# Optimization experiments

Measured on AMD Instinct MI355X. Metric: run time of the kernel, lower is better.

## Reference

```python
import jax, jax.numpy as jnp
import numpy as np

NUM_HEADS = 16


def setup_inputs() -> dict:
    key = jax.random.key(0)
    ks = jax.random.split(key, 5)
    N, L, E = 4, 1024, 1024
    x = jax.random.normal(ks[0], (N, L, E), dtype=jnp.float32)
    sc = 1.0 / np.sqrt(E)
    wq = jax.random.normal(ks[1], (E, E), dtype=jnp.float32) * sc
    wk = jax.random.normal(ks[2], (E, E), dtype=jnp.float32) * sc
    wv = jax.random.normal(ks[3], (E, E), dtype=jnp.float32) * sc
    wo = jax.random.normal(ks[4], (E, E), dtype=jnp.float32) * sc
    return {"x": x, "wq": wq, "wk": wk, "wv": wv, "wo": wo}


def reference(x, wq, wk, wv, wo):
    N, L, E = x.shape
    H = NUM_HEADS
    d = E // H  # d_k = d_v = d_q
    # Linear layers: y = x @ W^T (torch Linear weight is (out, in))
    q = (x @ wq.T).reshape(N, H, L, d)  # NOTE: raw view, matches torch .view
    k = (x @ wk.T).reshape(N, H, L, d)
    v = (x @ wv.T).reshape(N, H, L, d)
    scores = jnp.einsum("nhld,nhmd->nhlm", q, k) / jnp.sqrt(jnp.float32(d))
    # causal mask (dropout is identity in eval / p=0)
    causal = jnp.tril(jnp.ones((L, L), dtype=bool))
    scores = jnp.where(causal, scores, jnp.float32(-jnp.inf))
    attn = jax.nn.softmax(scores, axis=-1)
    wei = jnp.einsum("nhlm,nhmd->nhld", attn, v).reshape(N, L, H * d)
    return wei @ wo.T
```

## Files before the change

### kernel.cpp

```cpp
#include <hip/hip_runtime.h>
#include <hip/hip_bf16.h>

using bf16 = __hip_bfloat16;
typedef __attribute__((ext_vector_type(8))) short bf16x8;
typedef __attribute__((ext_vector_type(4))) float f32x4;

#define MFMA16(a, b, c) __builtin_amdgcn_mfma_f32_16x16x32_bf16(a, b, c, 0, 0, 0)
#define SWZ(row, byteoff) ((byteoff) ^ (((row) & 7) << 4))

__device__ __forceinline__ unsigned short f2b(float f) {
  union { float f; unsigned int u; } c; c.f = f;
  unsigned int r = c.u + 0x7fffu + ((c.u >> 16) & 1u);
  return (unsigned short)(r >> 16);
}
__device__ __forceinline__ float b2f(short b) {
  union { unsigned int u; float f; } c;
  c.u = ((unsigned int)(unsigned short)b) << 16;
  return c.f;
}
__device__ __forceinline__ bf16x8 scale8(bf16x8 v, float s) {
  bf16x8 r;
#pragma unroll
  for (int j = 0; j < 8; ++j) r[j] = (short)f2b(b2f(v[j]) * s);
  return r;
}

__device__ __forceinline__ void gload_lds16(const void* g, void* l) {
  __builtin_amdgcn_global_load_lds(
      (const __attribute__((address_space(1))) void*)g,
      (__attribute__((address_space(3))) void*)l, 16, 0, 0);
}

__device__ __forceinline__ void store_out(float* p, float v) { *p = v; }
__device__ __forceinline__ void store_out(bf16* p, float v) {
  *(unsigned short*)p = f2b(v);
}

__global__ __launch_bounds__(256) void cast_all(
    const float* __restrict__ x, const float* __restrict__ wq,
    const float* __restrict__ wk, const float* __restrict__ wv,
    const float* __restrict__ wo,
    unsigned short* __restrict__ xb, unsigned short* __restrict__ wqb,
    unsigned short* __restrict__ wkb, unsigned short* __restrict__ wvb,
    unsigned short* __restrict__ wob) {
  int i = blockIdx.x * 256 + threadIdx.x;
  const float* src;
  unsigned short* dst;
  int off;
  if (i < 1048576) {
    src = x; dst = xb; off = i;
  } else {
    int j = i - 1048576;
    int seg = j >> 18;
    off = j & 262143;
    src = (seg == 0) ? wq : (seg == 1) ? wk : (seg == 2) ? wv : wo;
    dst = (seg == 0) ? wqb : (seg == 1) ? wkb : (seg == 2) ? wvb : wob;
  }
  float4 v = reinterpret_cast<const float4*>(src)[off];
  ushort4 o;
  o.x = f2b(v.x); o.y = f2b(v.y); o.z = f2b(v.z); o.w = f2b(v.w);
  reinterpret_cast<ushort4*>(dst)[off] = o;
}

template <typename TOUT>
__device__ __forceinline__ void gemm_tile(const bf16* __restrict__ A,
                                          const bf16* __restrict__ Bt,
                                          TOUT* __restrict__ C, int N, int K,
                                          int bm, int bn) {
  __shared__ bf16 Asm[128 * 32];
  __shared__ bf16 Bsm[128 * 32];
  const int tid = threadIdx.x;
  const int lane = tid & 63;
  const int w = tid >> 6;
  const int wr = w >> 1, wc = w & 1;
  const int fr = lane & 15;
  const int fk = (lane >> 4) * 8;
  f32x4 acc[4][4] = {};

  const int srow = w * 16 + (lane >> 2);
  const int scol = (lane & 3) * 8;
  const bf16* Ag = A + (size_t)(bm + srow) * K + scol;
  const bf16* Bg = Bt + (size_t)srow * K + scol;
  bf16* AsW = &Asm[(w * 16) * 32];
  bf16* BsW = &Bsm[(w * 16) * 32];

  for (int kt = 0; kt < K; kt += 32) {
    gload_lds16(Ag + kt, AsW);
    gload_lds16(Ag + kt + (size_t)64 * K, AsW + 64 * 32);
    gload_lds16(Bg + kt, BsW);
    gload_lds16(Bg + kt + (size_t)64 * K, BsW + 64 * 32);
    __syncthreads();
    bf16x8 afr[4], bfr[4];
#pragma unroll
    for (int m = 0; m < 4; ++m)
      afr[m] = *(const bf16x8*)&Asm[(wr * 64 + m * 16 + fr) * 32 + fk];
#pragma unroll
    for (int n = 0; n < 4; ++n)
      bfr[n] = *(const bf16x8*)&Bsm[(wc * 64 + n * 16 + fr) * 32 + fk];
#pragma unroll
    for (int m = 0; m < 4; ++m)
#pragma unroll
      for (int n = 0; n < 4; ++n)
        acc[m][n] = MFMA16(afr[m], bfr[n], acc[m][n]);
    __syncthreads();
  }
#pragma unroll
  for (int m = 0; m < 4; ++m) {
    const int row0 = bm + wr * 64 + m * 16 + (lane >> 4) * 4;
#pragma unroll
    for (int n = 0; n < 4; ++n) {
      const int col = bn + wc * 64 + n * 16 + fr;
#pragma unroll
      for (int r = 0; r < 4; ++r)
        store_out(&C[(size_t)(row0 + r) * N + col], acc[m][n][r]);
    }
  }
}

__global__ __launch_bounds__(256) void gemm_qkv(
    const bf16* __restrict__ A, const bf16* __restrict__ B3,
    bf16* __restrict__ Cq, bf16* __restrict__ Ck, bf16* __restrict__ Cv) {
  const int bm = blockIdx.x * 128;
  const int bnG = blockIdx.y * 128;
  bf16* C = (bnG < 1024) ? Cq : (bnG < 2048) ? Ck : Cv;
  gemm_tile<bf16>(A, B3 + (size_t)bnG * 1024, C, 1024, 1024, bm, bnG & 1023);
}

__global__ __launch_bounds__(256) void gemm_out(const bf16* __restrict__ A,
                                                const bf16* __restrict__ B,
                                                float* __restrict__ C) {
  gemm_tile<float>(A, B + (size_t)blockIdx.y * 128 * 1024, C, 1024, 1024,
                   blockIdx.x * 128, blockIdx.y * 128);
}

__global__ __launch_bounds__(256) void attn_fwd(
    const bf16* __restrict__ Q, const bf16* __restrict__ K,
    const bf16* __restrict__ V, bf16* __restrict__ O) {
  const int nh = blockIdx.y;
  const size_t base = (size_t)nh * 65536;
  const bf16* Qp = Q + base;
  const bf16* Kp = K + base;
  const bf16* Vp = V + base;
  bf16* Op = O + base;
  const int p = blockIdx.x;
  const int qiA = p, qiB = 15 - p;
  const int tid = threadIdx.x;
  const int lane = tid & 63;
  const int w = tid >> 6;
  const int fr = lane & 15;
  const int fg = lane >> 4;

  __shared__ bf16 Ksm[2][64 * 64];
  __shared__ bf16 Vts[2][64 * 64];
  __shared__ bf16 Psm[4][2][16 * 64];

  const float QSC = 0.125f * 1.44269504089f;
  const float MS = 12.0f;
  const int rA0 = qiA * 64 + w * 16;
  const int rB0 = qiB * 64 + w * 16;
  bf16x8 qA[2], qB[2];
#pragma unroll
  for (int ks = 0; ks < 2; ++ks) {
    qA[ks] = scale8(
        *(const bf16x8*)&Qp[(size_t)(rA0 + fr) * 64 + ks * 32 + fg * 8], QSC);
    qB[ks] = scale8(
        *(const bf16x8*)&Qp[(size_t)(rB0 + fr) * 64 + ks * 32 + fg * 8], QSC);
  }

  float sA[4] = {0.f, 0.f, 0.f, 0.f};
  float sB[4] = {0.f, 0.f, 0.f, 0.f};
  f32x4 oA[4], oB[4];
#pragma unroll
  for (int d = 0; d < 4; ++d) {
    oA[d] = (f32x4){0.f, 0.f, 0.f, 0.f};
    oB[d] = (f32x4){0.f, 0.f, 0.f, 0.f};
  }

  const int NKV = qiB + 1;

  const int bkv = (tid & 15) * 4;
  const int bd = (tid >> 4) * 4;
  union VU { ushort4 v; unsigned short s[4]; };
  VU v4[4], nv4[4];

  const int krow = w * 16 + (lane >> 3);
  const int kcb = (lane & 7) * 16;

#define STAGE_K(kt, bi)                                                       \
  {                                                                           \
    _Pragma("unroll") for (int i = 0; i < 2; ++i) {                           \
      const int row = krow + i * 8;                                           \
      gload_lds16((const char*)Kp + ((size_t)((kt)*64 + row) * 128 +          \
                                     SWZ(row, kcb)),                          \
                  (char*)&Ksm[bi][0] + (w * 16 + i * 8) * 128);               \
    }                                                                         \
  }
#define LOAD_V(kt, r)                                                         \
  {                                                                           \
    _Pragma("unroll") for (int j = 0; j < 4; ++j) (r)[j].v =                  \
        *(const ushort4*)(Vp + (size_t)((kt)*64 + bkv + j) * 64 + bd);        \
  }
#define WRITE_V(bi, r)                                                        \
  {                                                                           \
    _Pragma("unroll") for (int i = 0; i < 4; ++i) {                           \
      VU o4;                                                                  \
      _Pragma("unroll") for (int j = 0; j < 4; ++j) o4.s[j] = (r)[j].s[i];    \
      const int row = bd + i;                                                 \
      *(ushort4*)((char*)&Vts[bi][0] + row * 128 + SWZ(row, bkv * 2)) = o4.v; \
    }                                                                         \
  }

  STAGE_K(0, 0);
  LOAD_V(0, v4);
  WRITE_V(0, v4);
  __syncthreads();

  for (int kt = 0; kt < NKV; ++kt) {
    const int b = kt & 1;
    const bool more = (kt + 1 < NKV);
    if (more) {
      STAGE_K(kt + 1, b ^ 1);
      LOAD_V(kt + 1, nv4);
    }
    const bool aAct = (kt <= qiA);

    bf16x8 kf[4][2];
#pragma unroll
    for (int c = 0; c < 4; ++c) {
      const int row = c * 16 + fr;
      const char* rp = (const char*)&Ksm[b][0] + row * 128;
      kf[c][0] = *(const bf16x8*)(rp + SWZ(row, fg * 16));
      kf[c][1] = *(const bf16x8*)(rp + SWZ(row, 64 + fg * 16));
    }

    auto strip_sm = [&](const bf16x8 (&qf)[2], float (&s)[4], bf16* Pw,
                        bool diag, int qrow0, bf16x8 (&pf)[2]) {
      f32x4 sc[4];
      __builtin_amdgcn_s_setprio(1);
#pragma unroll
      for (int c = 0; c < 4; ++c) {
        f32x4 acc = (f32x4){0.f, 0.f, 0.f, 0.f};
        acc = MFMA16(qf[0], kf[c][0], acc);
        acc = MFMA16(qf[1], kf[c][1], acc);
        sc[c] = acc;
      }
      __builtin_amdgcn_s_setprio(0);
#pragma unroll
      for (int c = 0; c < 4; ++c)
#pragma unroll
        for (int r = 0; r < 4; ++r) {
          float sv = sc[c][r];
          if (diag) {
            const int kcol = c * 16 + fr;
            const int qrow = qrow0 + r;
            sv = (kcol <= qrow) ? sv : -INFINITY;
          }
          const float e = __builtin_amdgcn_exp2f(sv - MS);
          s[r] += e;
          const int row = fg * 4 + r;
          *(unsigned short*)((char*)Pw + row * 128 +
                             SWZ(row, (c * 16 + fr) * 2)) = f2b(e);
        }
#pragma unroll
      for (int ks = 0; ks < 2; ++ks)
        pf[ks] = *(const bf16x8*)((char*)Pw + fr * 128 +
                                  SWZ(fr, ks * 64 + fg * 16));
    };

    bf16x8 pfA[2], pfB[2];
    strip_sm(qB, sB, &Psm[w][1][0], kt == qiB, w * 16 + fg * 4, pfB);
    if (aAct) strip_sm(qA, sA, &Psm[w][0][0], kt == qiA, w * 16 + fg * 4, pfA);

    bf16x8 vf[4][2];
#pragma unroll
    for (int d = 0; d < 4; ++d) {
      const int row = d * 16 + fr;
      const char* rp = (const char*)&Vts[b][0] + row * 128;
      vf[d][0] = *(const bf16x8*)(rp + SWZ(row, fg * 16));
      vf[d][1] = *(const bf16x8*)(rp + SWZ(row, 64 + fg * 16));
    }
    __builtin_amdgcn_s_setprio(1);
#pragma unroll
    for (int d = 0; d < 4; ++d) {
      oB[d] = MFMA16(pfB[0], vf[d][0], oB[d]);
      oB[d] = MFMA16(pfB[1], vf[d][1], oB[d]);
    }
    if (aAct) {
#pragma unroll
      for (int d = 0; d < 4; ++d) {
        oA[d] = MFMA16(pfA[0], vf[d][0], oA[d]);
        oA[d] = MFMA16(pfA[1], vf[d][1], oA[d]);
      }
    }
    __builtin_amdgcn_s_setprio(0);

    if (more) WRITE_V(b ^ 1, nv4);
    __syncthreads();
  }

#pragma unroll
  for (int msk = 1; msk <= 8; msk <<= 1)
#pragma unroll
    for (int r = 0; r < 4; ++r) {
      sA[r] += __shfl_xor(sA[r], msk);
      sB[r] += __shfl_xor(sB[r], msk);
    }

#pragma unroll
  for (int d = 0; d < 4; ++d)
#pragma unroll
    for (int r = 0; r < 4; ++r) {
      const float vA = oA[d][r] / sA[r];
      const float vB = oB[d][r] / sB[r];
      *(unsigned short*)&Op[(size_t)(rA0 + fg * 4 + r) * 64 + d * 16 + fr] =
          f2b(vA);
      *(unsigned short*)&Op[(size_t)(rB0 + fg * 4 + r) * 64 + d * 16 + fr] =
          f2b(vB);
    }
#undef STAGE_K
#undef LOAD_V
#undef WRITE_V
}

extern "C" void kernel_launch(void* const* d_in, const int* in_sizes, int n_in,
                              void* d_out, int out_size, void* d_ws,
                              size_t ws_size, hipStream_t stream) {
  const float* x = (const float*)d_in[0];
  const float* wq = (const float*)d_in[1];
  const float* wk = (const float*)d_in[2];
  const float* wv = (const float*)d_in[3];
  const float* wo = (const float*)d_in[4];
  float* out = (float*)d_out;
  char* ws = (char*)d_ws;

  bf16* xb = (bf16*)(ws);
  bf16* wqkv = (bf16*)(ws + (8u << 20));
  bf16* wqb = wqkv;
  bf16* wkb = (bf16*)(ws + (10u << 20));
  bf16* wvb = (bf16*)(ws + (12u << 20));
  bf16* wob = (bf16*)(ws + (14u << 20));
  bf16* qbuf = (bf16*)(ws + (16u << 20));
  bf16* kbuf = (bf16*)(ws + (24u << 20));
  bf16* vbuf = (bf16*)(ws + (32u << 20));
  bf16* weib = (bf16*)(ws);

  cast_all<<<8192, 256, 0, stream>>>(x, wq, wk, wv, wo, (unsigned short*)xb,
                                     (unsigned short*)wqb, (unsigned short*)wkb,
                                     (unsigned short*)wvb, (unsigned short*)wob);
  gemm_qkv<<<dim3(32, 24), 256, 0, stream>>>(xb, wqkv, qbuf, kbuf, vbuf);
  attn_fwd<<<dim3(8, 64), 256, 0, stream>>>(qbuf, kbuf, vbuf, weib);
  gemm_out<<<dim3(32, 8), 256, 0, stream>>>(weib, wob, out);
}
```

Measured before the change: 102.0 us.

## Replace QKV GEMM with 256x256-tile, 512-thread, triple-buffered pipelined kernel

The QKV projection now uses a new kernel with 256x256 output tiles, 8 waves per block and a 3-stage LDS ring fed by direct global-to-LDS loads. Waits use explicit vmcnt counts and raised MFMA priority so loads overlap compute. The larger tiles raise operand reuse and cut global traffic. In exchange the grid shrinks from 768 to 192 blocks on a GPU with many CUs, which risks poor occupancy and load balance, and LDS use grows to 96 KB per block.

```diff
diff --git a/kernel.cpp b/kernel.cpp
--- a/kernel.cpp
+++ b/kernel.cpp
@@ -7,6 +7,7 @@
 
 #define MFMA16(a, b, c) __builtin_amdgcn_mfma_f32_16x16x32_bf16(a, b, c, 0, 0, 0)
 #define SWZ(row, byteoff) ((byteoff) ^ (((row) & 7) << 4))
+#define SWZ64(row, byteoff) ((byteoff) ^ (((row) & 3) << 4))
 
 __device__ __forceinline__ unsigned short f2b(float f) {
   union { float f; unsigned int u; } c; c.f = f;
@@ -117,20 +118,116 @@
   }
 }
 
-__global__ __launch_bounds__(256) void gemm_qkv(
-    const bf16* __restrict__ A, const bf16* __restrict__ B3,
-    bf16* __restrict__ Cq, bf16* __restrict__ Ck, bf16* __restrict__ Cv) {
-  const int bm = blockIdx.x * 128;
-  const int bnG = blockIdx.y * 128;
-  bf16* C = (bnG < 1024) ? Cq : (bnG < 2048) ? Ck : Cv;
-  gemm_tile<bf16>(A, B3 + (size_t)bnG * 1024, C, 1024, 1024, bm, bnG & 1023);
-}
-
 __global__ __launch_bounds__(256) void gemm_out(const bf16* __restrict__ A,
                                                 const bf16* __restrict__ B,
                                                 float* __restrict__ C) {
   gemm_tile<float>(A, B + (size_t)blockIdx.y * 128 * 1024, C, 1024, 1024,
                    blockIdx.x * 128, blockIdx.y * 128);
+}
+
+__global__ __launch_bounds__(512, 2) void gemm_qkv_256(
+    const bf16* __restrict__ A, const bf16* __restrict__ B3,
+    bf16* __restrict__ Cq, bf16* __restrict__ Ck, bf16* __restrict__ Cv) {
+  __shared__ bf16 Ab[3][256 * 32];
+  __shared__ bf16 Bb[3][256 * 32];
+  const int tid = threadIdx.x;
+  const int lane = tid & 63;
+  const int w = tid >> 6;
+  const int wr = w >> 2;
+  const int wc = w & 3;
+  const int fr = lane & 15;
+  const int fg = lane >> 4;
+  const int bm = blockIdx.x * 256;
+  const int bnG = blockIdx.y * 256;
+  const bf16* Bt = B3 + (size_t)bnG * 1024;
+  bf16* C = (bnG < 1024) ? Cq : (bnG < 2048) ? Ck : Cv;
+  const int bn = bnG & 1023;
+
+  const int sr = w * 16 + (lane >> 2);
+  const int scb = (lane & 3) * 16;
+
+  f32x4 acc[8][4] = {};
+
+#define STAGE256(kt, s)                                                      \
+  {                                                                          \
+    const size_t kc = (size_t)(kt) * 32;                                     \
+    _Pragma("unroll") for (int ra = 0; ra < 2; ++ra) {                       \
+      const int row = ra * 128 + sr;                                         \
+      gload_lds16((const char*)(A + (size_t)(bm + row) * 1024 + kc) +        \
+                      SWZ64(row, scb),                                       \
+                  (char*)&Ab[s][0] + (ra * 128 + w * 16) * 64);              \
+      gload_lds16((const char*)(Bt + (size_t)row * 1024 + kc) +              \
+                      SWZ64(row, scb),                                       \
+                  (char*)&Bb[s][0] + (ra * 128 + w * 16) * 64);              \
+    }                                                                        \
+  }
+
+#define COMPUTE256(s)                                                        \
+  {                                                                          \
+    bf16x8 af[8];                                                            \
+    _Pragma("unroll") for (int m = 0; m < 8; ++m) {                          \
+      const int row = wr * 128 + m * 16 + fr;                                \
+      af[m] = *(const bf16x8*)((const char*)&Ab[s][0] + row * 64 +           \
+                               SWZ64(row, fg * 16));                         \
+    }                                                                        \
+    _Pragma("unroll") for (int nh = 0; nh < 2; ++nh) {                       \
+      bf16x8 bfv[2];                                                         \
+      _Pragma("unroll") for (int n = 0; n < 2; ++n) {                        \
+        const int row = wc * 64 + (nh * 2 + n) * 16 + fr;                    \
+        bfv[n] = *(const bf16x8*)((const char*)&Bb[s][0] + row * 64 +        \
+                                  SWZ64(row, fg * 16));                      \
+      }                                                                      \
+      __builtin_amdgcn_s_setprio(1);                                         \
+      _Pragma("unroll") for (int m = 0; m < 8; ++m)                          \
+          _Pragma("unroll") for (int n = 0; n < 2; ++n) acc[m][nh * 2 + n] = \
+              MFMA16(af[m], bfv[n], acc[m][nh * 2 + n]);                     \
+      __builtin_amdgcn_s_setprio(0);                                         \
+    }                                                                        \
+  }
+
+  STAGE256(0, 0);
+  STAGE256(1, 1);
+  STAGE256(2, 2);
+  __builtin_amdgcn_sched_barrier(0);
+  asm volatile("s_waitcnt vmcnt(8)" ::: "memory");
+  __builtin_amdgcn_s_barrier();
+  __builtin_amdgcn_sched_barrier(0);
+
+  int s = 0;
+  for (int t = 0; t < 32; ++t) {
+    COMPUTE256(s);
+    __builtin_amdgcn_sched_barrier(0);
+    __builtin_amdgcn_s_barrier();
+    __builtin_amdgcn_sched_barrier(0);
+    if (t + 3 < 32) {
+      STAGE256(t + 3, s);
+      __builtin_amdgcn_sched_barrier(0);
+      asm volatile("s_waitcnt vmcnt(8)" ::: "memory");
+    } else if (t + 2 < 32) {
+      asm volatile("s_waitcnt vmcnt(4)" ::: "memory");
+    } else if (t + 1 < 32) {
+      asm volatile("s_waitcnt vmcnt(0)" ::: "memory");
+    }
+    if (t + 1 < 32) {
+      __builtin_amdgcn_s_barrier();
+      __builtin_amdgcn_sched_barrier(0);
+    }
+    s = (s == 2) ? 0 : s + 1;
+  }
+
+#pragma unroll
+  for (int m = 0; m < 8; ++m) {
+    const int row0 = bm + wr * 128 + m * 16 + fg * 4;
+#pragma unroll
+    for (int n = 0; n < 4; ++n) {
+      const int col = bn + wc * 64 + n * 16 + fr;
+#pragma unroll
+      for (int r = 0; r < 4; ++r)
+        store_out(&C[(size_t)(row0 + r) * 1024 + col], acc[m][n][r]);
+    }
+  }
+#undef STAGE256
+#undef COMPUTE256
 }
 
 __global__ __launch_bounds__(256) void attn_fwd(
@@ -347,7 +444,7 @@
   cast_all<<<8192, 256, 0, stream>>>(x, wq, wk, wv, wo, (unsigned short*)xb,
                                      (unsigned short*)wqb, (unsigned short*)wkb,
                                      (unsigned short*)wvb, (unsigned short*)wob);
-  gemm_qkv<<<dim3(32, 24), 256, 0, stream>>>(xb, wqkv, qbuf, kbuf, vbuf);
+  gemm_qkv_256<<<dim3(16, 12), 512, 0, stream>>>(xb, wqkv, qbuf, kbuf, vbuf);
   attn_fwd<<<dim3(8, 64), 256, 0, stream>>>(qbuf, kbuf, vbuf, weib);
   gemm_out<<<dim3(32, 8), 256, 0, stream>>>(weib, wob, out);
 }
```

Result: slower. 115.9 us (+13.6%).

## Process four causal query strips per attention block to reuse K/V tiles

Applied to the files above, without the earlier changes.

Each attention block now handles four query strips (g, 7-g, 8+g, 15-g) instead of two, so every staged K/V tile in LDS feeds up to four strips' MFMAs. This halves the grid to 4x64 blocks and halves redundant K/V global loads per head, while keeping the causal work balanced across blocks. The cost is more registers per thread (four sets of Q fragments and accumulators), which the launch bound of one block per CU accommodates, and fewer blocks (256) to fill the GPU's CUs.

```diff
diff --git a/kernel.cpp b/kernel.cpp
--- a/kernel.cpp
+++ b/kernel.cpp
@@ -133,7 +133,7 @@
                    blockIdx.x * 128, blockIdx.y * 128);
 }
 
-__global__ __launch_bounds__(256) void attn_fwd(
+__global__ __launch_bounds__(256, 1) void attn_fwd(
     const bf16* __restrict__ Q, const bf16* __restrict__ K,
     const bf16* __restrict__ V, bf16* __restrict__ O) {
   const int nh = blockIdx.y;
@@ -142,8 +142,8 @@
   const bf16* Kp = K + base;
   const bf16* Vp = V + base;
   bf16* Op = O + base;
-  const int p = blockIdx.x;
-  const int qiA = p, qiB = 15 - p;
+  const int g = blockIdx.x;
+  const int strips[4] = {g, 7 - g, 8 + g, 15 - g};
   const int tid = threadIdx.x;
   const int lane = tid & 63;
   const int w = tid >> 6;
@@ -152,31 +152,32 @@
 
   __shared__ bf16 Ksm[2][64 * 64];
   __shared__ bf16 Vts[2][64 * 64];
-  __shared__ bf16 Psm[4][2][16 * 64];
+  __shared__ bf16 Psm[4][4][16 * 64];
 
   const float QSC = 0.125f * 1.44269504089f;
   const float MS = 12.0f;
-  const int rA0 = qiA * 64 + w * 16;
-  const int rB0 = qiB * 64 + w * 16;
-  bf16x8 qA[2], qB[2];
-#pragma unroll
-  for (int ks = 0; ks < 2; ++ks) {
-    qA[ks] = scale8(
-        *(const bf16x8*)&Qp[(size_t)(rA0 + fr) * 64 + ks * 32 + fg * 8], QSC);
-    qB[ks] = scale8(
-        *(const bf16x8*)&Qp[(size_t)(rB0 + fr) * 64 + ks * 32 + fg * 8], QSC);
-  }
-
-  float sA[4] = {0.f, 0.f, 0.f, 0.f};
-  float sB[4] = {0.f, 0.f, 0.f, 0.f};
-  f32x4 oA[4], oB[4];
-#pragma unroll
-  for (int d = 0; d < 4; ++d) {
-    oA[d] = (f32x4){0.f, 0.f, 0.f, 0.f};
-    oB[d] = (f32x4){0.f, 0.f, 0.f, 0.f};
-  }
-
-  const int NKV = qiB + 1;
+
+  bf16x8 qf[4][2];
+#pragma unroll
+  for (int si = 0; si < 4; ++si) {
+    const int r0 = strips[si] * 64 + w * 16;
+#pragma unroll
+    for (int ks = 0; ks < 2; ++ks)
+      qf[si][ks] = scale8(
+          *(const bf16x8*)&Qp[(size_t)(r0 + fr) * 64 + ks * 32 + fg * 8], QSC);
+  }
+
+  float sm[4][4];
+  f32x4 o[4][4];
+#pragma unroll
+  for (int si = 0; si < 4; ++si)
+#pragma unroll
+    for (int r = 0; r < 4; ++r) {
+      sm[si][r] = 0.f;
+      o[si][r] = (f32x4){0.f, 0.f, 0.f, 0.f};
+    }
+
+  const int NKV = strips[3] + 1;
 
   const int bkv = (tid & 15) * 4;
   const int bd = (tid >> 4) * 4;
@@ -222,7 +223,6 @@
       STAGE_K(kt + 1, b ^ 1);
       LOAD_V(kt + 1, nv4);
     }
-    const bool aAct = (kt <= qiA);
 
     bf16x8 kf[4][2];
 #pragma unroll
@@ -233,15 +233,15 @@
       kf[c][1] = *(const bf16x8*)(rp + SWZ(row, 64 + fg * 16));
     }
 
-    auto strip_sm = [&](const bf16x8 (&qf)[2], float (&s)[4], bf16* Pw,
+    auto strip_sm = [&](const bf16x8 (&qfs)[2], float (&s)[4], bf16* Pw,
                         bool diag, int qrow0, bf16x8 (&pf)[2]) {
       f32x4 sc[4];
       __builtin_amdgcn_s_setprio(1);
 #pragma unroll
       for (int c = 0; c < 4; ++c) {
         f32x4 acc = (f32x4){0.f, 0.f, 0.f, 0.f};
-        acc = MFMA16(qf[0], kf[c][0], acc);
-        acc = MFMA16(qf[1], kf[c][1], acc);
+        acc = MFMA16(qfs[0], kf[c][0], acc);
+        acc = MFMA16(qfs[1], kf[c][1], acc);
         sc[c] = acc;
       }
       __builtin_amdgcn_s_setprio(0);
@@ -267,9 +267,13 @@
                                   SWZ(fr, ks * 64 + fg * 16));
     };
 
-    bf16x8 pfA[2], pfB[2];
-    strip_sm(qB, sB, &Psm[w][1][0], kt == qiB, w * 16 + fg * 4, pfB);
-    if (aAct) strip_sm(qA, sA, &Psm[w][0][0], kt == qiA, w * 16 + fg * 4, pfA);
+    bf16x8 pf[4][2];
+    const int qrow0 = w * 16 + fg * 4;
+#pragma unroll
+    for (int si = 0; si < 4; ++si)
+      if (kt <= strips[si])
+        strip_sm(qf[si], sm[si], &Psm[w][si][0], kt == strips[si], qrow0,
+                 pf[si]);
 
     bf16x8 vf[4][2];
 #pragma unroll
@@ -281,17 +285,14 @@
     }
     __builtin_amdgcn_s_setprio(1);
 #pragma unroll
-    for (int d = 0; d < 4; ++d) {
-      oB[d] = MFMA16(pfB[0], vf[d][0], oB[d]);
-      oB[d] = MFMA16(pfB[1], vf[d][1], oB[d]);
-    }
-    if (aAct) {
-#pragma unroll
-      for (int d = 0; d < 4; ++d) {
-        oA[d] = MFMA16(pfA[0], vf[d][0], oA[d]);
-        oA[d] = MFMA16(pfA[1], vf[d][1], oA[d]);
+    for (int si = 0; si < 4; ++si)
+      if (kt <= strips[si]) {
+#pragma unroll
+        for (int d = 0; d < 4; ++d) {
+          o[si][d] = MFMA16(pf[si][0], vf[d][0], o[si][d]);
+          o[si][d] = MFMA16(pf[si][1], vf[d][1], o[si][d]);
+        }
       }
-    }
     __builtin_amdgcn_s_setprio(0);
 
     if (more) WRITE_V(b ^ 1, nv4);
@@ -301,22 +302,22 @@
 #pragma unroll
   for (int msk = 1; msk <= 8; msk <<= 1)
 #pragma unroll
-    for (int r = 0; r < 4; ++r) {
-      sA[r] += __shfl_xor(sA[r], msk);
-      sB[r] += __shfl_xor(sB[r], msk);
-    }
-
-#pragma unroll
-  for (int d = 0; d < 4; ++d)
-#pragma unroll
-    for (int r = 0; r < 4; ++r) {
-      const float vA = oA[d][r] / sA[r];
-      const float vB = oB[d][r] / sB[r];
-      *(unsigned short*)&Op[(size_t)(rA0 + fg * 4 + r) * 64 + d * 16 + fr] =
-          f2b(vA);
-      *(unsigned short*)&Op[(size_t)(rB0 + fg * 4 + r) * 64 + d * 16 + fr] =
-          f2b(vB);
-    }
+    for (int si = 0; si < 4; ++si)
+#pragma unroll
+      for (int r = 0; r < 4; ++r) sm[si][r] += __shfl_xor(sm[si][r], msk);
+
+#pragma unroll
+  for (int si = 0; si < 4; ++si) {
+    const int r0 = strips[si] * 64 + w * 16;
+#pragma unroll
+    for (int d = 0; d < 4; ++d)
+#pragma unroll
+      for (int r = 0; r < 4; ++r) {
+        const float val = o[si][d][r] / sm[si][r];
+        *(unsigned short*)&Op[(size_t)(r0 + fg * 4 + r) * 64 + d * 16 + fr] =
+            f2b(val);
+      }
+  }
 #undef STAGE_K
 #undef LOAD_V
 #undef WRITE_V
@@ -348,6 +349,6 @@
                                      (unsigned short*)wqb, (unsigned short*)wkb,
                                      (unsigned short*)wvb, (unsigned short*)wob);
   gemm_qkv<<<dim3(32, 24), 256, 0, stream>>>(xb, wqkv, qbuf, kbuf, vbuf);
-  attn_fwd<<<dim3(8, 64), 256, 0, stream>>>(qbuf, kbuf, vbuf, weib);
+  attn_fwd<<<dim3(4, 64), 256, 0, stream>>>(qbuf, kbuf, vbuf, weib);
   gemm_out<<<dim3(32, 8), 256, 0, stream>>>(weib, wob, out);
 }
```

New measurement: 108.3 us. +6.1%, slower.

## Keep attention probabilities in registers via transposed QK^T and swizzle GEMM block order

Applied to the files above, without the earlier changes.

The score MFMA is computed as K·Q^T so each lane holds probabilities along the kv dimension, which match the A-operand layout for the PV MFMA. The P tile can then be packed with v_cvt_pk_bf16_f32 directly in registers instead of round-tripping through shared memory. The V fragment loads are rearranged into two 8-byte reads to match that permuted kv ordering. Row sums are reduced per lane and redistributed with shuffles at the end. Separately, both GEMMs remap block indices in a strided swizzle to improve L2 reuse of A and B tiles.

```diff
diff --git a/kernel.cpp b/kernel.cpp
--- a/kernel.cpp
+++ b/kernel.cpp
@@ -22,6 +22,11 @@
   bf16x8 r;
 #pragma unroll
   for (int j = 0; j < 8; ++j) r[j] = (short)f2b(b2f(v[j]) * s);
+  return r;
+}
+__device__ __forceinline__ unsigned cvtpk(float a, float b) {
+  unsigned r;
+  asm("v_cvt_pk_bf16_f32 %0, %1, %2" : "=v"(r) : "v"(a), "v"(b));
   return r;
 }
 
@@ -120,8 +125,10 @@
 __global__ __launch_bounds__(256) void gemm_qkv(
     const bf16* __restrict__ A, const bf16* __restrict__ B3,
     bf16* __restrict__ Cq, bf16* __restrict__ Ck, bf16* __restrict__ Cv) {
-  const int bm = blockIdx.x * 128;
-  const int bnG = blockIdx.y * 128;
+  const int id = blockIdx.y * 32 + blockIdx.x;
+  const int sw = (id & 7) * 96 + (id >> 3);
+  const int bm = (sw & 31) * 128;
+  const int bnG = (sw >> 5) * 128;
   bf16* C = (bnG < 1024) ? Cq : (bnG < 2048) ? Ck : Cv;
   gemm_tile<bf16>(A, B3 + (size_t)bnG * 1024, C, 1024, 1024, bm, bnG & 1023);
 }
@@ -129,8 +136,11 @@
 __global__ __launch_bounds__(256) void gemm_out(const bf16* __restrict__ A,
                                                 const bf16* __restrict__ B,
                                                 float* __restrict__ C) {
-  gemm_tile<float>(A, B + (size_t)blockIdx.y * 128 * 1024, C, 1024, 1024,
-                   blockIdx.x * 128, blockIdx.y * 128);
+  const int id = blockIdx.y * 32 + blockIdx.x;
+  const int sw = (id & 7) * 32 + (id >> 3);
+  const int bm = (sw & 31) * 128;
+  const int bn = (sw >> 5) * 128;
+  gemm_tile<float>(A, B + (size_t)bn * 1024, C, 1024, 1024, bm, bn);
 }
 
 __global__ __launch_bounds__(256) void attn_fwd(
@@ -152,7 +162,6 @@
 
   __shared__ bf16 Ksm[2][64 * 64];
   __shared__ bf16 Vts[2][64 * 64];
-  __shared__ bf16 Psm[4][2][16 * 64];
 
   const float QSC = 0.125f * 1.44269504089f;
   const float MS = 12.0f;
@@ -167,8 +176,7 @@
         *(const bf16x8*)&Qp[(size_t)(rB0 + fr) * 64 + ks * 32 + fg * 8], QSC);
   }
 
-  float sA[4] = {0.f, 0.f, 0.f, 0.f};
-  float sB[4] = {0.f, 0.f, 0.f, 0.f};
+  float sA = 0.f, sB = 0.f;
   f32x4 oA[4], oB[4];
 #pragma unroll
   for (int d = 0; d < 4; ++d) {
@@ -177,6 +185,7 @@
   }
 
   const int NKV = qiB + 1;
+  const int qloc = w * 16 + fr;
 
   const int bkv = (tid & 15) * 4;
   const int bd = (tid >> 4) * 4;
@@ -215,6 +224,9 @@
   WRITE_V(0, v4);
   __syncthreads();
 
+  union PU { bf16x8 v; unsigned u[4]; };
+  union VF { bf16x8 v; unsigned long long q[2]; };
+
   for (int kt = 0; kt < NKV; ++kt) {
     const int b = kt & 1;
     const bool more = (kt + 1 < NKV);
@@ -232,64 +244,70 @@
       kf[c][0] = *(const bf16x8*)(rp + SWZ(row, fg * 16));
       kf[c][1] = *(const bf16x8*)(rp + SWZ(row, 64 + fg * 16));
     }
-
-    auto strip_sm = [&](const bf16x8 (&qf)[2], float (&s)[4], bf16* Pw,
-                        bool diag, int qrow0, bf16x8 (&pf)[2]) {
+    VF vf[4][2];
+#pragma unroll
+    for (int d = 0; d < 4; ++d) {
+      const int row = d * 16 + fr;
+      const char* rp = (const char*)&Vts[b][0] + row * 128;
+#pragma unroll
+      for (int ks = 0; ks < 2; ++ks) {
+        vf[d][ks].q[0] =
+            *(const unsigned long long*)(rp + SWZ(row, ks * 64 + fg * 8));
+        vf[d][ks].q[1] =
+            *(const unsigned long long*)(rp + SWZ(row, ks * 64 + 32 + fg * 8));
+      }
+    }
+
+    auto strip_sm = [&](const bf16x8 (&qf)[2], float& s, bool diag,
+                        PU (&pa)[2]) {
       f32x4 sc[4];
       __builtin_amdgcn_s_setprio(1);
 #pragma unroll
       for (int c = 0; c < 4; ++c) {
         f32x4 acc = (f32x4){0.f, 0.f, 0.f, 0.f};
-        acc = MFMA16(qf[0], kf[c][0], acc);
-        acc = MFMA16(qf[1], kf[c][1], acc);
+        acc = MFMA16(kf[c][0], qf[0], acc);
+        acc = MFMA16(kf[c][1], qf[1], acc);
         sc[c] = acc;
       }
       __builtin_amdgcn_s_setprio(0);
+      float pv[4][4];
 #pragma unroll
       for (int c = 0; c < 4; ++c)
 #pragma unroll
         for (int r = 0; r < 4; ++r) {
           float sv = sc[c][r];
           if (diag) {
-            const int kcol = c * 16 + fr;
-            const int qrow = qrow0 + r;
-            sv = (kcol <= qrow) ? sv : -INFINITY;
+            const int kvloc = c * 16 + fg * 4 + r;
+            sv = (kvloc <= qloc) ? sv : -INFINITY;
           }
           const float e = __builtin_amdgcn_exp2f(sv - MS);
-          s[r] += e;
-          const int row = fg * 4 + r;
-          *(unsigned short*)((char*)Pw + row * 128 +
-                             SWZ(row, (c * 16 + fr) * 2)) = f2b(e);
+          pv[c][r] = e;
+          s += e;
         }
 #pragma unroll
-      for (int ks = 0; ks < 2; ++ks)
-        pf[ks] = *(const bf16x8*)((char*)Pw + fr * 128 +
-                                  SWZ(fr, ks * 64 + fg * 16));
+      for (int ks = 0; ks < 2; ++ks) {
+        pa[ks].u[0] = cvtpk(pv[ks * 2][0], pv[ks * 2][1]);
+        pa[ks].u[1] = cvtpk(pv[ks * 2][2], pv[ks * 2][3]);
+        pa[ks].u[2] = cvtpk(pv[ks * 2 + 1][0], pv[ks * 2 + 1][1]);
+        pa[ks].u[3] = cvtpk(pv[ks * 2 + 1][2], pv[ks * 2 + 1][3]);
+      }
     };
 
-    bf16x8 pfA[2], pfB[2];
-    strip_sm(qB, sB, &Psm[w][1][0], kt == qiB, w * 16 + fg * 4, pfB);
-    if (aAct) strip_sm(qA, sA, &Psm[w][0][0], kt == qiA, w * 16 + fg * 4, pfA);
-
-    bf16x8 vf[4][2];
+    PU paA[2], paB[2];
+    strip_sm(qB, sB, kt == qiB, paB);
+    if (aAct) strip_sm(qA, sA, kt == qiA, paA);
+
+    __builtin_amdgcn_s_setprio(1);
 #pragma unroll
     for (int d = 0; d < 4; ++d) {
-      const int row = d * 16 + fr;
-      const char* rp = (const char*)&Vts[b][0] + row * 128;
-      vf[d][0] = *(const bf16x8*)(rp + SWZ(row, fg * 16));
-      vf[d][1] = *(const bf16x8*)(rp + SWZ(row, 64 + fg * 16));
-    }
-    __builtin_amdgcn_s_setprio(1);
-#pragma unroll
-    for (int d = 0; d < 4; ++d) {
-      oB[d] = MFMA16(pfB[0], vf[d][0], oB[d]);
-      oB[d] = MFMA16(pfB[1], vf[d][1], oB[d]);
+      oB[d] = MFMA16(paB[0].v, vf[d][0].v, oB[d]);
+      oB[d] = MFMA16(paB[1].v, vf[d][1].v, oB[d]);
     }
     if (aAct) {
 #pragma unroll
       for (int d = 0; d < 4; ++d) {
-        oA[d] = MFMA16(pfA[0], vf[d][0], oA[d]);
-        oA[d] = MFMA16(pfA[1], vf[d][1], oA[d]);
+        oA[d] = MFMA16(paA[0].v, vf[d][0].v, oA[d]);
+        oA[d] = MFMA16(paA[1].v, vf[d][1].v, oA[d]);
       }
     }
     __builtin_amdgcn_s_setprio(0);
@@ -298,20 +316,21 @@
     __syncthreads();
   }
 
-#pragma unroll
-  for (int msk = 1; msk <= 8; msk <<= 1)
+  sA += __shfl_xor(sA, 16); sA += __shfl_xor(sA, 32);
+  sB += __shfl_xor(sB, 16); sB += __shfl_xor(sB, 32);
+  float sAo[4], sBo[4];
+#pragma unroll
+  for (int r = 0; r < 4; ++r) {
+    sAo[r] = __shfl(sA, fg * 4 + r);
+    sBo[r] = __shfl(sB, fg * 4 + r);
+  }
+
+#pragma unroll
+  for (int d = 0; d < 4; ++d)
 #pragma unroll
     for (int r = 0; r < 4; ++r) {
-      sA[r] += __shfl_xor(sA[r], msk);
-      sB[r] += __shfl_xor(sB[r], msk);
-    }
-
-#pragma unroll
-  for (int d = 0; d < 4; ++d)
-#pragma unroll
-    for (int r = 0; r < 4; ++r) {
-      const float vA = oA[d][r] / sA[r];
-      const float vB = oB[d][r] / sB[r];
+      const float vA = oA[d][r] / sAo[r];
+      const float vB = oB[d][r] / sBo[r];
       *(unsigned short*)&Op[(size_t)(rA0 + fg * 4 + r) * 64 + d * 16 + fr] =
           f2b(vA);
       *(unsigned short*)&Op[(size_t)(rB0 + fg * 4 + r) * 64 + d * 16 + fr] =
```

After: 103.4 us. Within noise of the previous version (+1.3%).
